# Kernel optimization log

Measured on AMD Instinct MI355X. Metric: run time of the kernel, lower is better.

Reference implementation:

```python
import jax, jax.numpy as jnp
import numpy as np

N = 100000        # nodes
E = 1600000       # edges
IN_NODE = 32
HID = 64
IN_EDGE = 8
OUT = 1


def setup_inputs() -> dict:
    key = jax.random.key(0)
    ks = jax.random.split(key, 16)

    def lin(k, fan_in, fan_out):
        s = 1.0 / np.sqrt(fan_in)
        kw, kb = jax.random.split(k)
        W = jax.random.uniform(kw, (fan_in, fan_out), jnp.float32, -s, s)
        b = jax.random.uniform(kb, (fan_out,), jnp.float32, -s, s)
        return W, b

    x = jax.random.normal(ks[0], (N, IN_NODE), jnp.float32)
    edge_index = jax.random.randint(ks[1], (2, E), 0, N, jnp.int64)
    edge_feat = jax.random.normal(ks[2], (E, IN_EDGE), jnp.float32)

    W0, b0 = lin(ks[3], IN_NODE, HID)        # gcn_in
    W1, b1 = lin(ks[4], HID, HID)            # gcn layer 1
    W2, b2 = lin(ks[5], HID, HID)            # gcn layer 2
    Wm1, bm1 = lin(ks[6], HID * 2 + IN_EDGE, HID)
    Wm2, bm2 = lin(ks[7], HID, HID // 2)
    Wm3, bm3 = lin(ks[8], HID // 2, OUT)

    return {"x": x, "edge_index": edge_index, "edge_feat": edge_feat,
            "W0": W0, "b0": b0, "W1": W1, "b1": b1, "W2": W2, "b2": b2,
            "Wm1": Wm1, "bm1": bm1, "Wm2": Wm2, "bm2": bm2, "Wm3": Wm3, "bm3": bm3}


def _gcn_conv(h, W, b, u, v, dinv):
    # PyG GCNConv: linear transform, symmetric-normalized aggregation with
    # self-loops, then bias. dinv = deg^{-1/2} with deg including self-loop.
    hW = h @ W                                       # [N, F]
    norm = (dinv[u] * dinv[v])[:, None]              # [E, 1]
    agg = jax.ops.segment_sum(hW[u] * norm, v, num_segments=N)
    agg = agg + hW * (dinv * dinv)[:, None]          # self-loop contribution
    return agg + b


def reference(x, edge_index, edge_feat, W0, b0, W1, b1, W2, b2, Wm1, bm1, Wm2, bm2, Wm3, bm3):
    u, v = edge_index[0], edge_index[1]
    # degree of target nodes, including added self-loops
    deg = jax.ops.segment_sum(jnp.ones((E,), x.dtype), v, num_segments=N) + 1.0
    dinv = jax.lax.rsqrt(deg)

    h = jax.nn.relu(_gcn_conv(x, W0, b0, u, v, dinv))
    h = jax.nn.relu(_gcn_conv(h, W1, b1, u, v, dinv))
    h = jax.nn.relu(_gcn_conv(h, W2, b2, u, v, dinv))

    # edge MLP: gather endpoints, concat with edge features
    z = jnp.concatenate([h[u], h[v], edge_feat], axis=-1)   # [E, 2*HID+IN_EDGE]
    z = jax.nn.relu(z @ Wm1 + bm1)
    z = jax.nn.relu(z @ Wm2 + bm2)
    return z @ Wm3 + bm3                                    # [E, OUT]
```

## Files before the change

### kernel.cpp

```cpp
#include <hip/hip_runtime.h>
#include <hip/hip_fp16.h>
#include <cstdint>

#define TPB 256
#define CHUNK 8192
#define BKTCAP 4096

typedef _Float16 h2 __attribute__((ext_vector_type(2)));

__device__ __forceinline__ float fdot2(h2 a, h2 b, float c) {
  return __builtin_amdgcn_fdot2(a, b, c, false);
}


__device__ __forceinline__ void fma_row64(float zi, const float* __restrict__ wrow,
                                          float* acc) {
  const float4* w4 = (const float4*)wrow;
#pragma unroll
  for (int j4 = 0; j4 < 16; ++j4) {
    float4 w = w4[j4];
    acc[4 * j4 + 0] = fmaf(zi, w.x, acc[4 * j4 + 0]);
    acc[4 * j4 + 1] = fmaf(zi, w.y, acc[4 * j4 + 1]);
    acc[4 * j4 + 2] = fmaf(zi, w.z, acc[4 * j4 + 2]);
    acc[4 * j4 + 3] = fmaf(zi, w.w, acc[4 * j4 + 3]);
  }
}

__global__ __launch_bounds__(TPB) void prep(int* __restrict__ gcnt, int nbkt,
                                            int n, const int* __restrict__ ei,
                                            int* __restrict__ flag,
                                            const float* __restrict__ x,
                                            __half* __restrict__ xh) {
  int i = blockIdx.x * TPB + threadIdx.x;
  if (i < nbkt) gcnt[i] = 0;
  if (i < n) {
    const float4* x4 = (const float4*)(x + (size_t)i * 32);
    __half2* o = (__half2*)(xh + (size_t)i * 32);
#pragma unroll
    for (int j = 0; j < 8; ++j) {
      float4 v = x4[j];
      o[2 * j + 0] = __floats2half2_rn(v.x, v.y);
      o[2 * j + 1] = __floats2half2_rn(v.z, v.w);
    }
  }
  if (i == 0) {
    int o = 0;
    for (int k = 0; k < 32; ++k) o |= ei[2 * k + 1];
    *flag = (o == 0) ? 1 : 0;
  }
}

__global__ __launch_bounds__(TPB) void passA(const int* __restrict__ ei,
                                             const int* __restrict__ flag,
                                             int* __restrict__ gcnt,
                                             uint32_t* __restrict__ bkt_buf,
                                             int E, int NBKT) {
  __shared__ int base0[1024], cur[1024], s4[TPB];
  __shared__ uint32_t stage[CHUNK];
  int tid = threadIdx.x;
  int start = blockIdx.x * CHUNK;
  int nloc = E - start;
  if (nloc > CHUNK) nloc = CHUNK;
  for (int i = tid; i < NBKT; i += TPB) cur[i] = 0;
  __syncthreads();
  bool f64 = (*flag != 0);
  for (int i = tid; i < nloc; i += TPB) {
    int e = start + i;
    int v = f64 ? ei[2 * ((size_t)E + e)] : ei[(size_t)E + e];
    atomicAdd(&cur[v >> 7], 1);
  }
  __syncthreads();
  int b0i = 4 * tid;
  int c0 = (b0i + 0 < NBKT) ? cur[b0i + 0] : 0;
  int c1 = (b0i + 1 < NBKT) ? cur[b0i + 1] : 0;
  int c2 = (b0i + 2 < NBKT) ? cur[b0i + 2] : 0;
  int c3 = (b0i + 3 < NBKT) ? cur[b0i + 3] : 0;
  int s = c0 + c1 + c2 + c3;
  s4[tid] = s;
  __syncthreads();
  for (int off = 1; off < TPB; off <<= 1) {
    int xv = (tid >= off) ? s4[tid - off] : 0;
    __syncthreads();
    s4[tid] += xv;
    __syncthreads();
  }
  int excl = s4[tid] - s;
  if (b0i + 0 < NBKT) base0[b0i + 0] = excl;
  if (b0i + 1 < NBKT) base0[b0i + 1] = excl + c0;
  if (b0i + 2 < NBKT) base0[b0i + 2] = excl + c0 + c1;
  if (b0i + 3 < NBKT) base0[b0i + 3] = excl + c0 + c1 + c2;
  __syncthreads();
  for (int i = tid; i < NBKT; i += TPB) cur[i] = base0[i];
  __syncthreads();
  for (int i = tid; i < nloc; i += TPB) {
    int e = start + i;
    int u, v;
    if (f64) { u = ei[2 * (size_t)e]; v = ei[2 * ((size_t)E + e)]; }
    else     { u = ei[e];             v = ei[(size_t)E + e]; }
    int b = v >> 7;
    int slot = atomicAdd(&cur[b], 1);
    stage[slot] = ((uint32_t)u << 7) | (uint32_t)(v & 127);
  }
  __syncthreads();
  for (int b = tid; b < NBKT; b += TPB) {
    int s0 = base0[b];
    int c = cur[b] - s0;
    if (c > 0) {
      int g = atomicAdd(&gcnt[b], c);
      int cc = min(c, max(0, BKTCAP - g));
      uint32_t* dst = bkt_buf + (size_t)b * BKTCAP + g;
      for (int i = 0; i < cc; ++i) dst[i] = stage[s0 + i];
    }
  }
}

__global__ void scanB(const int* __restrict__ gcnt, int* __restrict__ bkt_base,
                      int* __restrict__ row_ptr, int NBKT, int N,
                      const float* __restrict__ W1e, const float* __restrict__ Wm2,
                      h2* __restrict__ w1p, h2* __restrict__ w2p) {
  __shared__ int tot[1024];
  int t = threadIdx.x;
  int s = (t < NBKT) ? min(gcnt[t], BKTCAP) : 0;
  tot[t] = s;
  __syncthreads();
  for (int off = 1; off < 1024; off <<= 1) {
    int x = (t >= off) ? tot[t - off] : 0;
    __syncthreads();
    tot[t] += x;
    __syncthreads();
  }
  if (t < NBKT) bkt_base[t] = tot[t] - s;
  if (t == 0) row_ptr[N] = tot[1023];
  if (t < 256) {
    int j = t >> 2, kk = t & 3;
    w1p[t] =
        h2{(_Float16)W1e[(2 * kk) * 64 + j], (_Float16)W1e[(2 * kk + 1) * 64 + j]};
  }
  if (t < 1024) {
    int j = t >> 5, kk = t & 31;
    w2p[t] =
        h2{(_Float16)Wm2[(2 * kk) * 32 + j], (_Float16)Wm2[(2 * kk + 1) * 32 + j]};
  }
}

__global__ __launch_bounds__(TPB) void passB(const uint32_t* __restrict__ bkt_buf,
                                             const int* __restrict__ gcnt,
                                             const int* __restrict__ bkt_base,
                                             int* __restrict__ row_ptr,
                                             float* __restrict__ dinv,
                                             int* __restrict__ u_sorted, int N) {
  int b = blockIdx.x;
  __shared__ int cnt128[128], offs128[128];
  int tid = threadIdx.x;
  if (tid < 128) cnt128[tid] = 0;
  __syncthreads();
  int m = min(gcnt[b], BKTCAP);
  const uint32_t* p = bkt_buf + (size_t)b * BKTCAP;
  for (int i = tid; i < m; i += TPB) atomicAdd(&cnt128[p[i] & 127], 1);
  __syncthreads();
  if (tid == 0) {
    int run = 0;
    for (int i = 0; i < 128; ++i) { offs128[i] = run; run += cnt128[i]; }
  }
  __syncthreads();
  int base = bkt_base[b];
  int node = b * 128 + tid;
  if (tid < 128 && node < N) {
    row_ptr[node] = base + offs128[tid];
    dinv[node] = rsqrtf((float)cnt128[tid] + 1.0f);
  }
  if (tid < 128) cnt128[tid] = 0;
  __syncthreads();
  for (int i = tid; i < m; i += TPB) {
    uint32_t pk = p[i];
    int vloc = pk & 127;
    int slot = base + offs128[vloc] + atomicAdd(&cnt128[vloc], 1);
    u_sorted[slot] = (int)(pk >> 7);
  }
}

__global__ __launch_bounds__(TPB) void aggregate32h(const __half* __restrict__ X,
                                                    const int* __restrict__ u_sorted,
                                                    const int* __restrict__ row_ptr,
                                                    const float* __restrict__ dinv,
                                                    float* __restrict__ xagg, int n) {
  int wave = (blockIdx.x * TPB + threadIdx.x) >> 6;
  int lane = threadIdx.x & 63;
  int q = lane >> 4, f2 = lane & 15;
  int node = wave * 4 + q;
  bool valid = node < n;
  int rs = 0, re = 0;
  float dv = 0.f;
  if (valid) { rs = row_ptr[node]; re = row_ptr[node + 1]; dv = dinv[node]; }
  const __half2* selfp = (const __half2*)(X + (size_t)(valid ? node : 0) * 32);
  float2 sf = __half22float2(selfp[f2]);
  float2 acc0 = make_float2(sf.x * dv, sf.y * dv);
  float2 acc1 = make_float2(0.f, 0.f);
  int sb = q << 4;
  for (int base = rs; base < re; base += 16) {
    int m = re - base;
    if (m > 16) m = 16;
    int uj = 0;
    float wj = 0.f;
    if (f2 < m) { uj = u_sorted[base + f2]; wj = dinv[uj]; }
    int k = 0;
    for (; k + 1 < m; k += 2) {
      int u0 = __shfl(uj, sb + k), u1 = __shfl(uj, sb + k + 1);
      float w0 = __shfl(wj, sb + k), w1 = __shfl(wj, sb + k + 1);
      float2 v0 = __half22float2(((const __half2*)(X + (size_t)u0 * 32))[f2]);
      float2 v1 = __half22float2(((const __half2*)(X + (size_t)u1 * 32))[f2]);
      acc0.x = fmaf(v0.x, w0, acc0.x);
      acc0.y = fmaf(v0.y, w0, acc0.y);
      acc1.x = fmaf(v1.x, w1, acc1.x);
      acc1.y = fmaf(v1.y, w1, acc1.y);
    }
    if (k < m) {
      int u0 = __shfl(uj, sb + k);
      float w0 = __shfl(wj, sb + k);
      float2 v0 = __half22float2(((const __half2*)(X + (size_t)u0 * 32))[f2]);
      acc0.x = fmaf(v0.x, w0, acc0.x);
      acc0.y = fmaf(v0.y, w0, acc0.y);
    }
  }
  if (valid) {
    float2 r = make_float2(dv * (acc0.x + acc1.x), dv * (acc0.y + acc1.y));
    ((float2*)(xagg + (size_t)node * 32))[f2] = r;
  }
}

__global__ __launch_bounds__(TPB) void lin32_64(const float* __restrict__ A,
                                                const float* __restrict__ W0,
                                                const float* __restrict__ b0v,
                                                const float* __restrict__ W1,
                                                __half* __restrict__ Bh, int n) {
  __shared__ __align__(16) float W0s[32 * 64];
  __shared__ __align__(16) float W1s[64 * 64];
  __shared__ float bs[64];
  int tid = threadIdx.x;
  for (int i = tid; i < 32 * 64; i += TPB) W0s[i] = W0[i];
  for (int i = tid; i < 64 * 64; i += TPB) W1s[i] = W1[i];
  if (tid < 64) bs[tid] = b0v[tid];
  __syncthreads();
  int node = blockIdx.x * TPB + tid;
  if (node >= n) return;
  const float4* a4 = (const float4*)(A + (size_t)node * 32);
  float h1[64];
#pragma unroll
  for (int j = 0; j < 64; ++j) h1[j] = bs[j];
  for (int i4 = 0; i4 < 8; ++i4) {
    float4 z = a4[i4];
    fma_row64(z.x, &W0s[(4 * i4 + 0) * 64], h1);
    fma_row64(z.y, &W0s[(4 * i4 + 1) * 64], h1);
    fma_row64(z.z, &W0s[(4 * i4 + 2) * 64], h1);
    fma_row64(z.w, &W0s[(4 * i4 + 3) * 64], h1);
  }
#pragma unroll
  for (int j = 0; j < 64; ++j) h1[j] = fmaxf(h1[j], 0.f);
  __half2* o2 = (__half2*)(Bh + (size_t)node * 64);
#pragma unroll
  for (int hf = 0; hf < 2; ++hf) {
    float acc[32];
#pragma unroll
    for (int j = 0; j < 32; ++j) acc[j] = 0.f;
    for (int i = 0; i < 64; ++i) {
      float zi = h1[i];
      const float4* w4 = (const float4*)&W1s[i * 64 + hf * 32];
#pragma unroll
      for (int j4 = 0; j4 < 8; ++j4) {
        float4 w = w4[j4];
        acc[4 * j4 + 0] = fmaf(zi, w.x, acc[4 * j4 + 0]);
        acc[4 * j4 + 1] = fmaf(zi, w.y, acc[4 * j4 + 1]);
        acc[4 * j4 + 2] = fmaf(zi, w.z, acc[4 * j4 + 2]);
        acc[4 * j4 + 3] = fmaf(zi, w.w, acc[4 * j4 + 3]);
      }
    }
#pragma unroll
    for (int j2 = 0; j2 < 16; ++j2)
      o2[hf * 16 + j2] = __floats2half2_rn(acc[2 * j2 + 0], acc[2 * j2 + 1]);
  }
}

__global__ __launch_bounds__(TPB) void lin_node64h(const float* __restrict__ A,
                                                   const float* __restrict__ W,
                                                   __half* __restrict__ Bh, int n) {
  __shared__ __align__(16) float Ws[64 * 64];
  int tid = threadIdx.x;
  for (int i = tid; i < 64 * 64; i += TPB) Ws[i] = W[i];
  __syncthreads();
  int node = blockIdx.x * TPB + tid;
  if (node >= n) return;
  const float4* a4 = (const float4*)(A + (size_t)node * 64);
  float acc[64];
#pragma unroll
  for (int j = 0; j < 64; ++j) acc[j] = 0.f;
  for (int i4 = 0; i4 < 16; ++i4) {
    float4 z = a4[i4];
    fma_row64(z.x, &Ws[(4 * i4 + 0) * 64], acc);
    fma_row64(z.y, &Ws[(4 * i4 + 1) * 64], acc);
    fma_row64(z.z, &Ws[(4 * i4 + 2) * 64], acc);
    fma_row64(z.w, &Ws[(4 * i4 + 3) * 64], acc);
  }
  __half2* o2 = (__half2*)(Bh + (size_t)node * 64);
#pragma unroll
  for (int j2 = 0; j2 < 32; ++j2)
    o2[j2] = __floats2half2_rn(acc[2 * j2 + 0], acc[2 * j2 + 1]);
}

__global__ __launch_bounds__(TPB) void aggregateh(const __half* __restrict__ Bh,
                                                  const int* __restrict__ u_sorted,
                                                  const int* __restrict__ row_ptr,
                                                  const float* __restrict__ dinv,
                                                  const float* __restrict__ bias,
                                                  float* __restrict__ A, int n) {
  int wave = (blockIdx.x * TPB + threadIdx.x) >> 6;
  int lane = threadIdx.x & 63;
  int half = lane >> 5, f2 = lane & 31;
  int node = wave * 2 + half;
  bool valid = node < n;
  int rs = 0, re = 0;
  float dv = 0.f;
  if (valid) { rs = row_ptr[node]; re = row_ptr[node + 1]; dv = dinv[node]; }
  const __half2* selfp = (const __half2*)(Bh + (size_t)(valid ? node : 0) * 64);
  float2 sf = __half22float2(selfp[f2]);
  float2 acc0 = make_float2(sf.x * dv, sf.y * dv);
  float2 acc1 = make_float2(0.f, 0.f);
  float2 acc2 = make_float2(0.f, 0.f);
  float2 acc3 = make_float2(0.f, 0.f);
  int sb = half << 5;
  for (int base = rs; base < re; base += 32) {
    int m = re - base;
    if (m > 32) m = 32;
    int uj = 0;
    float wj = 0.f;
    if (f2 < m) { uj = u_sorted[base + f2]; wj = dinv[uj]; }
    int k = 0;
    for (; k + 3 < m; k += 4) {
      int u0 = __shfl(uj, sb + k), u1 = __shfl(uj, sb + k + 1);
      int u2 = __shfl(uj, sb + k + 2), u3 = __shfl(uj, sb + k + 3);
      float w0 = __shfl(wj, sb + k), w1 = __shfl(wj, sb + k + 1);
      float w2 = __shfl(wj, sb + k + 2), w3 = __shfl(wj, sb + k + 3);
      float2 v0 = __half22float2(((const __half2*)(Bh + (size_t)u0 * 64))[f2]);
      float2 v1 = __half22float2(((const __half2*)(Bh + (size_t)u1 * 64))[f2]);
      float2 v2 = __half22float2(((const __half2*)(Bh + (size_t)u2 * 64))[f2]);
      float2 v3 = __half22float2(((const __half2*)(Bh + (size_t)u3 * 64))[f2]);
      acc0.x = fmaf(v0.x, w0, acc0.x); acc0.y = fmaf(v0.y, w0, acc0.y);
      acc1.x = fmaf(v1.x, w1, acc1.x); acc1.y = fmaf(v1.y, w1, acc1.y);
      acc2.x = fmaf(v2.x, w2, acc2.x); acc2.y = fmaf(v2.y, w2, acc2.y);
      acc3.x = fmaf(v3.x, w3, acc3.x); acc3.y = fmaf(v3.y, w3, acc3.y);
    }
    for (; k < m; ++k) {
      int u0 = __shfl(uj, sb + k);
      float w0 = __shfl(wj, sb + k);
      float2 v0 = __half22float2(((const __half2*)(Bh + (size_t)u0 * 64))[f2]);
      acc0.x = fmaf(v0.x, w0, acc0.x);
      acc0.y = fmaf(v0.y, w0, acc0.y);
    }
  }
  if (valid) {
    float2 bi = ((const float2*)bias)[f2];
    float2 r;
    r.x = fmaxf(dv * ((acc0.x + acc1.x) + (acc2.x + acc3.x)) + bi.x, 0.f);
    r.y = fmaxf(dv * ((acc0.y + acc1.y) + (acc2.y + acc3.y)) + bi.y, 0.f);
    ((float2*)(A + (size_t)node * 64))[f2] = r;
  }
}

__global__ __launch_bounds__(TPB) void lin_ab(const float* __restrict__ A,
                                              const float* __restrict__ W,
                                              __half* __restrict__ apre,
                                              __half* __restrict__ bpre, int n) {
  __shared__ __align__(16) float Ws[128 * 64];
  int tid = threadIdx.x;
  for (int i = tid; i < 128 * 64; i += TPB) Ws[i] = W[i];
  __syncthreads();
  int node = blockIdx.x * TPB + tid;
  if (node >= n) return;
  const float4* a4 = (const float4*)(A + (size_t)node * 64);
  float acc[64];
#pragma unroll
  for (int j = 0; j < 64; ++j) acc[j] = 0.f;
  for (int i4 = 0; i4 < 16; ++i4) {
    float4 z = a4[i4];
    fma_row64(z.x, &Ws[(4 * i4 + 0) * 64], acc);
    fma_row64(z.y, &Ws[(4 * i4 + 1) * 64], acc);
    fma_row64(z.z, &Ws[(4 * i4 + 2) * 64], acc);
    fma_row64(z.w, &Ws[(4 * i4 + 3) * 64], acc);
  }
  __half2* o2 = (__half2*)(apre + (size_t)node * 64);
#pragma unroll
  for (int j2 = 0; j2 < 32; ++j2)
    o2[j2] = __floats2half2_rn(acc[2 * j2 + 0], acc[2 * j2 + 1]);
#pragma unroll
  for (int j = 0; j < 64; ++j) acc[j] = 0.f;
  for (int i4 = 0; i4 < 16; ++i4) {
    float4 z = a4[i4];
    fma_row64(z.x, &Ws[(64 + 4 * i4 + 0) * 64], acc);
    fma_row64(z.y, &Ws[(64 + 4 * i4 + 1) * 64], acc);
    fma_row64(z.z, &Ws[(64 + 4 * i4 + 2) * 64], acc);
    fma_row64(z.w, &Ws[(64 + 4 * i4 + 3) * 64], acc);
  }
  o2 = (__half2*)(bpre + (size_t)node * 64);
#pragma unroll
  for (int j2 = 0; j2 < 32; ++j2)
    o2[j2] = __floats2half2_rn(acc[2 * j2 + 0], acc[2 * j2 + 1]);
}

__global__ __launch_bounds__(TPB) void edge_mlp(
    const __half* __restrict__ apre, const __half* __restrict__ bpre,
    const int* __restrict__ ei, const int* __restrict__ flag,
    const float* __restrict__ EF, const h2* __restrict__ w1p,
    const float* __restrict__ bm1, const h2* __restrict__ w2p,
    const float* __restrict__ bm2, const float* __restrict__ Wm3,
    const float* __restrict__ bm3, float* __restrict__ out, int E) {
  int e = blockIdx.x * TPB + threadIdx.x;
  if (e >= E) return;
  int u, v;
  if (*flag) {
    u = ei[2 * (size_t)e];
    v = ei[2 * ((size_t)E + e)];
  } else {
    u = ei[e];
    v = ei[(size_t)E + e];
  }
  const h2* a2 = (const h2*)(apre + (size_t)u * 64);
  const h2* b2 = (const h2*)(bpre + (size_t)v * 64);
  const float4* ef4 = (const float4*)(EF + (size_t)e * 8);
  float4 z0 = ef4[0], z1 = ef4[1];
  h2 efh[4];
  efh[0] = h2{(_Float16)z0.x, (_Float16)z0.y};
  efh[1] = h2{(_Float16)z0.z, (_Float16)z0.w};
  efh[2] = h2{(_Float16)z1.x, (_Float16)z1.y};
  efh[3] = h2{(_Float16)z1.z, (_Float16)z1.w};
  const h2 selLo = h2{(_Float16)1.f, (_Float16)0.f};
  const h2 selHi = h2{(_Float16)0.f, (_Float16)1.f};

  float acc[64];
#pragma unroll
  for (int j = 0; j < 64; ++j) {
    h2 sel = (j & 1) ? selHi : selLo;
    float a = fdot2(a2[j >> 1], sel, bm1[j]);
    a = fdot2(b2[j >> 1], sel, a);
    const h2* wp = w1p + j * 4;
    a = fdot2(efh[0], wp[0], a);
    a = fdot2(efh[1], wp[1], a);
    a = fdot2(efh[2], wp[2], a);
    a = fdot2(efh[3], wp[3], a);
    acc[j] = a;
  }

  h2 zh[32];
#pragma unroll
  for (int i2 = 0; i2 < 32; ++i2)
    zh[i2] = h2{(_Float16)fmaxf(acc[2 * i2 + 0], 0.f),
                (_Float16)fmaxf(acc[2 * i2 + 1], 0.f)};

  float o = bm3[0];
#pragma unroll
  for (int j = 0; j < 32; ++j) {
    float z = bm2[j];
    const h2* wp = w2p + j * 32;
#pragma unroll
    for (int kk = 0; kk < 32; ++kk) z = fdot2(zh[kk], wp[kk], z);
    o = fmaf(fmaxf(z, 0.f), Wm3[j], o);
  }
  out[e] = o;
}

extern "C" void kernel_launch(void* const* d_in, const int* in_sizes, int n_in,
                              void* d_out, int out_size, void* d_ws, size_t ws_size,
                              hipStream_t stream) {
  const float* x   = (const float*)d_in[0];
  const int*   ei  = (const int*)d_in[1];
  const float* ef  = (const float*)d_in[2];
  const float* W0  = (const float*)d_in[3];
  const float* b0  = (const float*)d_in[4];
  const float* W1  = (const float*)d_in[5];
  const float* b1  = (const float*)d_in[6];
  const float* W2  = (const float*)d_in[7];
  const float* b2  = (const float*)d_in[8];
  const float* Wm1 = (const float*)d_in[9];
  const float* bm1 = (const float*)d_in[10];
  const float* Wm2 = (const float*)d_in[11];
  const float* bm2 = (const float*)d_in[12];
  const float* Wm3 = (const float*)d_in[13];
  const float* bm3 = (const float*)d_in[14];
  float* out = (float*)d_out;

  const int N = in_sizes[0] / 32;
  const int E = in_sizes[2] / 8;
  const int NBKT = (N + 127) >> 7;

  char* p = (char*)d_ws;
  auto carve = [&](size_t bytes) {
    void* r = (void*)p;
    p += ((bytes + 255) / 256) * 256;
    return r;
  };
  int*      row_ptr  = (int*)carve((size_t)(N + 1) * 4);
  float*    dinv     = (float*)carve((size_t)N * 4);
  int*      flag     = (int*)carve(256);
  h2*       w1p      = (h2*)carve(256 * 4);
  h2*       w2p      = (h2*)carve(1024 * 4);
  int*      gcnt     = (int*)carve((size_t)NBKT * 4);
  int*      bkt_base = (int*)carve((size_t)(NBKT + 1) * 4);
  uint32_t* bkt_buf  = (uint32_t*)carve((size_t)NBKT * BKTCAP * 4);
  int*      u_sorted = (int*)carve((size_t)E * 4);
  float*    hA       = (float*)carve((size_t)N * 64 * 4);
  float*    hB       = (float*)carve((size_t)N * 64 * 4);
  __half*   linh     = (__half*)carve((size_t)N * 64 * 2);
  __half*   apreh    = (__half*)carve((size_t)N * 64 * 2);
  __half*   bpreh    = (__half*)carve((size_t)N * 64 * 2);
  if ((size_t)(p - (char*)d_ws) > ws_size) return;

  float* xagg = hB;
  __half* xh = apreh;

  const int EB = (E + TPB - 1) / TPB;
  const int NB = (N + TPB - 1) / TPB;
  const int EBC = (E + CHUNK - 1) / CHUNK;
  const int AB2 = (((N + 1) / 2) + 3) / 4;
  const int AB4 = (((N + 3) / 4) + 3) / 4;

  prep<<<NB, TPB, 0, stream>>>(gcnt, NBKT, N, ei, flag, x, xh);
  passA<<<EBC, TPB, 0, stream>>>(ei, flag, gcnt, bkt_buf, E, NBKT);
  scanB<<<1, 1024, 0, stream>>>(gcnt, bkt_base, row_ptr, NBKT, N,
                                Wm1 + 128 * 64, Wm2, w1p, w2p);
  passB<<<NBKT, TPB, 0, stream>>>(bkt_buf, gcnt, bkt_base, row_ptr, dinv,
                                  u_sorted, N);

  aggregate32h<<<AB4, TPB, 0, stream>>>(xh, u_sorted, row_ptr, dinv, xagg, N);
  lin32_64<<<NB, TPB, 0, stream>>>(xagg, W0, b0, W1, linh, N);
  aggregateh<<<AB2, TPB, 0, stream>>>(linh, u_sorted, row_ptr, dinv, b1, hB, N);
  lin_node64h<<<NB, TPB, 0, stream>>>(hB, W2, linh, N);
  aggregateh<<<AB2, TPB, 0, stream>>>(linh, u_sorted, row_ptr, dinv, b2, hA, N);

  lin_ab<<<NB, TPB, 0, stream>>>(hA, Wm1, apreh, bpreh, N);

  edge_mlp<<<EB, TPB, 0, stream>>>(apreh, bpreh, ei, flag, ef, w1p, bm1, w2p, bm2,
                                   Wm3, bm3, out, E);
}
```

Measured before the change: 400.7 us.

## Use MFMA for edge MLP second layer and pre-convert edge features to fp16

The edge MLP's 64x32 second layer was a per-thread loop of fdot2 calls. It now writes each wavefront's hidden activations to shared memory and runs them through 16x16x16 fp16 MFMA tiles, finishing the Wm3 projection with lane shuffles. Edge features are also converted to fp16 in the prep kernel, which now launches over E threads, so edge_mlp reads half the bytes. The cost is extra LDS use per block and a separate conversion pass that writes and re-reads the fp16 edge features.

Measured after the change: 423.7 us. 5.7% more time.

```diff
diff --git a/kernel.cpp b/kernel.cpp
--- a/kernel.cpp
+++ b/kernel.cpp
@@ -7,6 +7,8 @@
 #define BKTCAP 4096
 
 typedef _Float16 h2 __attribute__((ext_vector_type(2)));
+typedef _Float16 h4 __attribute__((ext_vector_type(4)));
+typedef float f4 __attribute__((ext_vector_type(4)));
 
 __device__ __forceinline__ float fdot2(h2 a, h2 b, float c) {
   return __builtin_amdgcn_fdot2(a, b, c, false);
@@ -30,7 +32,9 @@
                                             int n, const int* __restrict__ ei,
                                             int* __restrict__ flag,
                                             const float* __restrict__ x,
-                                            __half* __restrict__ xh) {
+                                            __half* __restrict__ xh,
+                                            const float* __restrict__ ef,
+                                            __half* __restrict__ efh, int E) {
   int i = blockIdx.x * TPB + threadIdx.x;
   if (i < nbkt) gcnt[i] = 0;
   if (i < n) {
@@ -42,6 +46,15 @@
       o[2 * j + 0] = __floats2half2_rn(v.x, v.y);
       o[2 * j + 1] = __floats2half2_rn(v.z, v.w);
     }
+  }
+  if (i < E) {
+    const float4* e4 = (const float4*)(ef + (size_t)i * 8);
+    float4 z0 = e4[0], z1 = e4[1];
+    __half2* o = (__half2*)(efh + (size_t)i * 8);
+    o[0] = __floats2half2_rn(z0.x, z0.y);
+    o[1] = __floats2half2_rn(z0.z, z0.w);
+    o[2] = __floats2half2_rn(z1.x, z1.y);
+    o[3] = __floats2half2_rn(z1.z, z1.w);
   }
   if (i == 0) {
     int o = 0;
@@ -117,7 +130,7 @@
 __global__ void scanB(const int* __restrict__ gcnt, int* __restrict__ bkt_base,
                       int* __restrict__ row_ptr, int NBKT, int N,
                       const float* __restrict__ W1e, const float* __restrict__ Wm2,
-                      h2* __restrict__ w1p, h2* __restrict__ w2p) {
+                      h2* __restrict__ w1p, __half* __restrict__ w2h) {
   __shared__ int tot[1024];
   int t = threadIdx.x;
   int s = (t < NBKT) ? min(gcnt[t], BKTCAP) : 0;
@@ -136,11 +149,7 @@
     w1p[t] =
         h2{(_Float16)W1e[(2 * kk) * 64 + j], (_Float16)W1e[(2 * kk + 1) * 64 + j]};
   }
-  if (t < 1024) {
-    int j = t >> 5, kk = t & 31;
-    w2p[t] =
-        h2{(_Float16)Wm2[(2 * kk) * 32 + j], (_Float16)Wm2[(2 * kk + 1) * 32 + j]};
-  }
+  for (int i = t; i < 2048; i += 1024) w2h[i] = __float2half(Wm2[i]);
 }
 
 __global__ __launch_bounds__(TPB) void passB(const uint32_t* __restrict__ bkt_buf,
@@ -408,29 +417,23 @@
 __global__ __launch_bounds__(TPB) void edge_mlp(
     const __half* __restrict__ apre, const __half* __restrict__ bpre,
     const int* __restrict__ ei, const int* __restrict__ flag,
-    const float* __restrict__ EF, const h2* __restrict__ w1p,
-    const float* __restrict__ bm1, const h2* __restrict__ w2p,
+    const __half* __restrict__ EFH, const h2* __restrict__ w1p,
+    const float* __restrict__ bm1, const __half* __restrict__ w2h,
     const float* __restrict__ bm2, const float* __restrict__ Wm3,
     const float* __restrict__ bm3, float* __restrict__ out, int E) {
-  int e = blockIdx.x * TPB + threadIdx.x;
-  if (e >= E) return;
+  __shared__ _Float16 stage[4][64][72];
+  int tid = threadIdx.x;
+  int wv = tid >> 6, l = tid & 63;
+  int e = blockIdx.x * TPB + tid;
+  bool valid = e < E;
+  int es = valid ? e : 0;
   int u, v;
-  if (*flag) {
-    u = ei[2 * (size_t)e];
-    v = ei[2 * ((size_t)E + e)];
-  } else {
-    u = ei[e];
-    v = ei[(size_t)E + e];
-  }
+  if (*flag) { u = ei[2 * (size_t)es]; v = ei[2 * ((size_t)E + es)]; }
+  else       { u = ei[es];             v = ei[(size_t)E + es]; }
   const h2* a2 = (const h2*)(apre + (size_t)u * 64);
   const h2* b2 = (const h2*)(bpre + (size_t)v * 64);
-  const float4* ef4 = (const float4*)(EF + (size_t)e * 8);
-  float4 z0 = ef4[0], z1 = ef4[1];
-  h2 efh[4];
-  efh[0] = h2{(_Float16)z0.x, (_Float16)z0.y};
-  efh[1] = h2{(_Float16)z0.z, (_Float16)z0.w};
-  efh[2] = h2{(_Float16)z1.x, (_Float16)z1.y};
-  efh[3] = h2{(_Float16)z1.z, (_Float16)z1.w};
+  const h2* ef2 = (const h2*)(EFH + (size_t)es * 8);
+  h2 efh[4] = {ef2[0], ef2[1], ef2[2], ef2[3]};
   const h2 selLo = h2{(_Float16)1.f, (_Float16)0.f};
   const h2 selHi = h2{(_Float16)0.f, (_Float16)1.f};
 
@@ -448,22 +451,61 @@
     acc[j] = a;
   }
 
-  h2 zh[32];
+  _Float16* srow = &stage[wv][l][0];
 #pragma unroll
   for (int i2 = 0; i2 < 32; ++i2)
-    zh[i2] = h2{(_Float16)fmaxf(acc[2 * i2 + 0], 0.f),
-                (_Float16)fmaxf(acc[2 * i2 + 1], 0.f)};
-
-  float o = bm3[0];
-#pragma unroll
-  for (int j = 0; j < 32; ++j) {
-    float z = bm2[j];
-    const h2* wp = w2p + j * 32;
-#pragma unroll
-    for (int kk = 0; kk < 32; ++kk) z = fdot2(zh[kk], wp[kk], z);
-    o = fmaf(fmaxf(z, 0.f), Wm3[j], o);
-  }
-  out[e] = o;
+    ((h2*)srow)[i2] = h2{(_Float16)fmaxf(acc[2 * i2 + 0], 0.f),
+                         (_Float16)fmaxf(acc[2 * i2 + 1], 0.f)};
+
+  int bcol = l & 15;
+  int brow = 4 * (l >> 4);
+  h4 bfr[2][4];
+#pragma unroll
+  for (int nn = 0; nn < 2; ++nn)
+#pragma unroll
+    for (int g = 0; g < 4; ++g) {
+      h4 t;
+#pragma unroll
+      for (int i = 0; i < 4; ++i)
+        t[i] = (_Float16)(((const _Float16*)w2h)[(g * 16 + brow + i) * 32 +
+                                                 nn * 16 + bcol]);
+      bfr[nn][g] = t;
+    }
+
+  const _Float16* wbase = &stage[wv][0][0];
+  f4 C[4][2] = {};
+#pragma unroll
+  for (int m = 0; m < 4; ++m) {
+    h4 afr[4];
+#pragma unroll
+    for (int g = 0; g < 4; ++g)
+      afr[g] = *(const h4*)(wbase + (m * 16 + bcol) * 72 + g * 16 + brow);
+#pragma unroll
+    for (int nn = 0; nn < 2; ++nn)
+#pragma unroll
+      for (int g = 0; g < 4; ++g)
+        C[m][nn] =
+            __builtin_amdgcn_mfma_f32_16x16x16f16(afr[g], bfr[nn][g], C[m][nn], 0, 0, 0);
+  }
+
+  float w3a = Wm3[bcol], w3b = Wm3[16 + bcol];
+  float c2a = bm2[bcol], c2b = bm2[16 + bcol];
+  float ob = bm3[0];
+  int ebase = blockIdx.x * TPB + wv * 64;
+#pragma unroll
+  for (int m = 0; m < 4; ++m) {
+#pragma unroll
+    for (int r = 0; r < 4; ++r) {
+      float p = fmaxf(C[m][0][r] + c2a, 0.f) * w3a +
+                fmaxf(C[m][1][r] + c2b, 0.f) * w3b;
+      p += __shfl_xor(p, 1);
+      p += __shfl_xor(p, 2);
+      p += __shfl_xor(p, 4);
+      p += __shfl_xor(p, 8);
+      int eo = ebase + m * 16 + 4 * (l >> 4) + r;
+      if (bcol == 0 && eo < E) out[eo] = p + ob;
+    }
+  }
 }
 
 extern "C" void kernel_launch(void* const* d_in, const int* in_sizes, int n_in,
@@ -500,7 +542,7 @@
   float*    dinv     = (float*)carve((size_t)N * 4);
   int*      flag     = (int*)carve(256);
   h2*       w1p      = (h2*)carve(256 * 4);
-  h2*       w2p      = (h2*)carve(1024 * 4);
+  __half*   w2h      = (__half*)carve(2048 * 2);
   int*      gcnt     = (int*)carve((size_t)NBKT * 4);
   int*      bkt_base = (int*)carve((size_t)(NBKT + 1) * 4);
   uint32_t* bkt_buf  = (uint32_t*)carve((size_t)NBKT * BKTCAP * 4);
@@ -510,6 +552,7 @@
   __half*   linh     = (__half*)carve((size_t)N * 64 * 2);
   __half*   apreh    = (__half*)carve((size_t)N * 64 * 2);
   __half*   bpreh    = (__half*)carve((size_t)N * 64 * 2);
+  __half*   efh16    = (__half*)carve((size_t)E * 8 * 2);
   if ((size_t)(p - (char*)d_ws) > ws_size) return;
 
   float* xagg = hB;
@@ -521,10 +564,10 @@
   const int AB2 = (((N + 1) / 2) + 3) / 4;
   const int AB4 = (((N + 3) / 4) + 3) / 4;
 
-  prep<<<NB, TPB, 0, stream>>>(gcnt, NBKT, N, ei, flag, x, xh);
+  prep<<<EB, TPB, 0, stream>>>(gcnt, NBKT, N, ei, flag, x, xh, ef, efh16, E);
   passA<<<EBC, TPB, 0, stream>>>(ei, flag, gcnt, bkt_buf, E, NBKT);
   scanB<<<1, 1024, 0, stream>>>(gcnt, bkt_base, row_ptr, NBKT, N,
-                                Wm1 + 128 * 64, Wm2, w1p, w2p);
+                                Wm1 + 128 * 64, Wm2, w1p, w2h);
   passB<<<NBKT, TPB, 0, stream>>>(bkt_buf, gcnt, bkt_base, row_ptr, dinv,
                                   u_sorted, N);
 
@@ -536,6 +579,6 @@
 
   lin_ab<<<NB, TPB, 0, stream>>>(hA, Wm1, apreh, bpreh, N);
 
-  edge_mlp<<<EB, TPB, 0, stream>>>(apreh, bpreh, ei, flag, ef, w1p, bm1, w2p, bm2,
-                                   Wm3, bm3, out, E);
-}
+  edge_mlp<<<EB, TPB, 0, stream>>>(apreh, bpreh, ei, flag, efh16, w1p, bm1, w2h,
+                                   bm2, Wm3, bm3, out, E);
+}
```
